# Optimization experiments

Hardware: AMD Instinct MI355X
Metric: run time of the kernel (lower is better)

## Reference

```python
import math
import jax
import jax.numpy as jnp
import numpy as np

N_NODE = 50000
N_EDGE = 1_600_000
D_IN = 128
D_K = 32
N_HEADS = 8


def setup_inputs() -> dict:
    key = jax.random.key(0)
    k_h, k_e, k_q, k_k, k_v = jax.random.split(key, 5)
    h = jax.random.normal(k_h, (N_NODE, D_IN), dtype=jnp.float32)
    edge_idx = jax.random.randint(k_e, (2, N_EDGE), 0, N_NODE, dtype=jnp.int64)
    scale = 1.0 / math.sqrt(D_IN)
    WQ = jax.random.normal(k_q, (N_HEADS, D_IN, D_K), dtype=jnp.float32) * scale
    WK = jax.random.normal(k_k, (N_HEADS, D_IN, D_K), dtype=jnp.float32) * scale
    WV = jax.random.normal(k_v, (N_HEADS, D_IN, D_K), dtype=jnp.float32) * scale
    return {"h": h, "edge_idx": edge_idx, "WQ": WQ, "WK": WK, "WV": WV}


def reference(h, edge_idx, WQ, WK, WV):
    n_node = h.shape[0]
    d_k = WK.shape[-1]
    # Per-head projections: [H, N, d]
    Q = jnp.einsum('nd,hdk->hnk', h, WQ)
    K = jnp.einsum('nd,hdk->hnk', h, WK)
    V = jnp.einsum('nd,hdv->hnv', h, WV)
    row = edge_idx[0]  # destination (softmax normalized per row, dim=1)
    col = edge_idx[1]  # source
    # Edge logits: e[h, e] = <Q[h, row[e]], K[h, col[e]]> / sqrt(d_k)
    e = jnp.einsum('hek,hek->he', Q[:, row, :], K[:, col, :]) / jnp.sqrt(
        jnp.asarray(d_k, dtype=h.dtype))
    eT = e.T  # [E, H]
    # Sparse (segment) softmax over outgoing edges of each row node.
    m = jax.ops.segment_max(eT, row, num_segments=n_node)  # [N, H]
    m = jnp.where(jnp.isfinite(m), m, jnp.zeros_like(m))   # guard empty rows
    ex = jnp.exp(eT - m[row])                               # [E, H]
    denom = jax.ops.segment_sum(ex, row, num_segments=n_node)  # [N, H]
    att = ex / denom[row]                                   # [E, H]
    # Sparse mm: out[i] = sum_{edges (i,j)} att * V[j]
    msgs = att[:, :, None] * jnp.transpose(V, (1, 0, 2))[col]  # [E, H, d_v]
    out = jax.ops.segment_sum(msgs, row, num_segments=n_node)  # [N, H, d_v]
    # aggregate == 'concat' -> head-major concat along feature dim
    return out.reshape(n_node, -1)
```

## Files before the change

### kernel.cpp

```cpp
#include <hip/hip_runtime.h>
#include <hip/hip_bf16.h>
#include <cstdint>

#define D_IN 128
#define DK 32
#define NH 8
#define HD 256

typedef __attribute__((ext_vector_type(8))) short short8;
typedef __attribute__((ext_vector_type(4))) float f32x4;

__device__ inline float bf2f(unsigned short u) {
  union { unsigned int i; float f; } c;
  c.i = ((unsigned int)u) << 16;
  return c.f;
}
__device__ inline short f2bf(float f) {
  union { float f; unsigned int i; } c; c.f = f;
  unsigned int u = c.i;
  u = u + 0x7FFFu + ((u >> 16) & 1u);
  return (short)(u >> 16);
}

__global__ __launch_bounds__(256) void prep_w_kernel(
    const float* __restrict__ WQ, const float* __restrict__ WK,
    const float* __restrict__ WV, short8* __restrict__ Bbuf) {
  int ct = blockIdx.x;
  int t = threadIdx.x;
  int kt = t >> 6, L = t & 63;
  int col = ct * 16 + (L & 15);
  int type = col >> 8;
  const float* W = (type == 0) ? WQ : (type == 1) ? WK : WV;
  int head = (col & 255) >> 5;
  int kk = col & 31;
  int k0 = kt * 32 + ((L >> 4) << 3);
  short8 o;
  #pragma unroll
  for (int r = 0; r < 8; r++)
    o[r] = f2bf(W[head * (D_IN * DK) + (k0 + r) * DK + kk]);
  Bbuf[(size_t)(ct * 4 + kt) * 64 + L] = o;
}

__global__ __launch_bounds__(256) void gemm_qkv_kernel(
    const float* __restrict__ h, const short8* __restrict__ Bbuf,
    __hip_bfloat16* __restrict__ Q, __hip_bfloat16* __restrict__ K,
    __hip_bfloat16* __restrict__ V, int nt_total) {
  __shared__ float hs[16][132];
  __shared__ short lds[16][768];
  int nt = blockIdx.x;
  int t = threadIdx.x;
  {
    const float4* h4 = (const float4*)(h + (size_t)nt * 16 * 128);
    float4 v0 = h4[t * 2], v1 = h4[t * 2 + 1];
    int node = t >> 4, dim = (t & 15) * 8;
    hs[node][dim + 0] = v0.x; hs[node][dim + 1] = v0.y;
    hs[node][dim + 2] = v0.z; hs[node][dim + 3] = v0.w;
    hs[node][dim + 4] = v1.x; hs[node][dim + 5] = v1.y;
    hs[node][dim + 6] = v1.z; hs[node][dim + 7] = v1.w;
  }
  __syncthreads();
  int w = t >> 6;
  int L = t & 63;
  int arow = L & 15, k0base = ((L >> 4) << 3);
  short8 afrag[4];
  #pragma unroll
  for (int kt = 0; kt < 4; kt++) {
    #pragma unroll
    for (int r = 0; r < 8; r++)
      afrag[kt][r] = f2bf(hs[arow][kt * 32 + k0base + r]);
  }
  f32x4 acc[12];
  #pragma unroll
  for (int c = 0; c < 12; c++) acc[c] = (f32x4){0.f, 0.f, 0.f, 0.f};
  #pragma unroll
  for (int kt = 0; kt < 4; kt++) {
    #pragma unroll
    for (int c = 0; c < 12; c++) {
      short8 b = Bbuf[(size_t)((w * 12 + c) * 4 + kt) * 64 + L];
      acc[c] = __builtin_amdgcn_mfma_f32_16x16x32_bf16(afrag[kt], b, acc[c], 0, 0, 0);
    }
  }
  int row0 = (L >> 4) << 2;
  int col0 = w * 192 + (L & 15);
  #pragma unroll
  for (int c = 0; c < 12; c++) {
    #pragma unroll
    for (int r = 0; r < 4; r++)
      lds[row0 + r][col0 + c * 16] = f2bf(acc[c][r]);
  }
  __syncthreads();
  __hip_bfloat16* dst[3] = {Q, K, V};
  #pragma unroll
  for (int s = 0; s < 3; s++) {
    char* base = (char*)(dst[s] + (size_t)nt * 16 * HD);
    #pragma unroll
    for (int j = 0; j < 2; j++) {
      int u = t + j * 256;
      int row = u >> 5, uc = u & 31;
      float4 vdat = *(const float4*)((const char*)&lds[row][0] + s * 512 + uc * 16);
      *(float4*)(base + row * 512 + uc * 16) = vdat;
    }
  }
}

__global__ void rank_kernel(const int* __restrict__ row, int n_edge,
                            int* __restrict__ cnt, int* __restrict__ rank) {
  int i = blockIdx.x * blockDim.x + threadIdx.x;
  if (i < n_edge) rank[i] = atomicAdd(&cnt[row[i]], 1);
}

__global__ __launch_bounds__(256) void scan1_kernel(
    const int* __restrict__ cnt, int n, int* __restrict__ exc,
    int* __restrict__ bsum) {
  __shared__ int s[256];
  int gid = blockIdx.x * 256 + threadIdx.x;
  int v = (gid < n) ? cnt[gid] : 0;
  s[threadIdx.x] = v;
  __syncthreads();
  #pragma unroll
  for (int off = 1; off < 256; off <<= 1) {
    int t = (threadIdx.x >= off) ? s[threadIdx.x - off] : 0;
    __syncthreads();
    s[threadIdx.x] += t;
    __syncthreads();
  }
  if (gid < n) exc[gid] = s[threadIdx.x] - v;
  if (threadIdx.x == 255) bsum[blockIdx.x] = s[255];
}

__global__ __launch_bounds__(256) void scan2_kernel(int* __restrict__ bsum,
                                                    int nb) {
  __shared__ int s[256];
  int v = (threadIdx.x < nb) ? bsum[threadIdx.x] : 0;
  s[threadIdx.x] = v;
  __syncthreads();
  #pragma unroll
  for (int off = 1; off < 256; off <<= 1) {
    int t = (threadIdx.x >= off) ? s[threadIdx.x - off] : 0;
    __syncthreads();
    s[threadIdx.x] += t;
    __syncthreads();
  }
  if (threadIdx.x < nb) bsum[threadIdx.x] = s[threadIdx.x] - v;
}

__global__ __launch_bounds__(256) void scan3_kernel(
    int* __restrict__ exc, const int* __restrict__ bsum, int n, int n_edge) {
  int gid = blockIdx.x * 256 + threadIdx.x;
  if (gid < n) exc[gid] = exc[gid] + bsum[blockIdx.x];
  if (gid == 0) exc[n] = n_edge;
}

__global__ void scatter_kernel(const int* __restrict__ row,
                               const int* __restrict__ col,
                               const int* __restrict__ rank, int n_edge,
                               const int* __restrict__ offsets,
                               int* __restrict__ col_sorted) {
  int i = blockIdx.x * blockDim.x + threadIdx.x;
  if (i < n_edge) col_sorted[offsets[row[i]] + rank[i]] = col[i];
}

__global__ __launch_bounds__(256) void attn_kernel(
    const __hip_bfloat16* __restrict__ Q, const __hip_bfloat16* __restrict__ K,
    const __hip_bfloat16* __restrict__ V, const int* __restrict__ offsets,
    const int* __restrict__ col_sorted, float* __restrict__ out, int n_node) {
  int wave = threadIdx.x >> 6;
  int lane = threadIdx.x & 63;
  int node = blockIdx.x * 4 + wave;
  if (node >= n_node) return;
  int start = offsets[node], end = offsets[node + 1];
  int d0 = lane * 4;

  float q0, q1, q2, q3;
  {
    ushort4 qv = *(const ushort4*)(Q + (size_t)node * HD + d0);
    q0 = bf2f(qv.x); q1 = bf2f(qv.y); q2 = bf2f(qv.z); q3 = bf2f(qv.w);
  }
  float m = -INFINITY, denom = 0.f;
  float a0 = 0.f, a1 = 0.f, a2 = 0.f, a3 = 0.f;

  for (int e = start; e < end; e += 2) {
    int c0 = col_sorted[e];
    bool has1 = (e + 1 < end);
    int c1 = has1 ? col_sorted[e + 1] : c0;
    ushort4 k0 = *(const ushort4*)(K + (size_t)c0 * HD + d0);
    ushort4 v0 = *(const ushort4*)(V + (size_t)c0 * HD + d0);
    ushort4 k1 = *(const ushort4*)(K + (size_t)c1 * HD + d0);
    ushort4 v1 = *(const ushort4*)(V + (size_t)c1 * HD + d0);
    {
      float d = q0 * bf2f(k0.x) + q1 * bf2f(k0.y) + q2 * bf2f(k0.z) +
                q3 * bf2f(k0.w);
      d += __shfl_xor(d, 1);
      d += __shfl_xor(d, 2);
      d += __shfl_xor(d, 4);
      float lg = d * 0.17677669529663687f;
      float nm = fmaxf(m, lg);
      float sc = __expf(m - nm);
      float p = __expf(lg - nm);
      denom = denom * sc + p;
      a0 = a0 * sc + p * bf2f(v0.x);
      a1 = a1 * sc + p * bf2f(v0.y);
      a2 = a2 * sc + p * bf2f(v0.z);
      a3 = a3 * sc + p * bf2f(v0.w);
      m = nm;
    }
    if (has1) {
      float d = q0 * bf2f(k1.x) + q1 * bf2f(k1.y) + q2 * bf2f(k1.z) +
                q3 * bf2f(k1.w);
      d += __shfl_xor(d, 1);
      d += __shfl_xor(d, 2);
      d += __shfl_xor(d, 4);
      float lg = d * 0.17677669529663687f;
      float nm = fmaxf(m, lg);
      float sc = __expf(m - nm);
      float p = __expf(lg - nm);
      denom = denom * sc + p;
      a0 = a0 * sc + p * bf2f(v1.x);
      a1 = a1 * sc + p * bf2f(v1.y);
      a2 = a2 * sc + p * bf2f(v1.z);
      a3 = a3 * sc + p * bf2f(v1.w);
      m = nm;
    }
  }
  float inv = (end > start) ? 1.f / denom : 0.f;
  float4 o = make_float4(a0 * inv, a1 * inv, a2 * inv, a3 * inv);
  *(float4*)(out + (size_t)node * HD + d0) = o;
}

extern "C" void kernel_launch(void* const* d_in, const int* in_sizes, int n_in,
                              void* d_out, int out_size, void* d_ws,
                              size_t ws_size, hipStream_t stream) {
  const float* h = (const float*)d_in[0];
  const int* edge = (const int*)d_in[1];
  const float* WQ = (const float*)d_in[2];
  const float* WK = (const float*)d_in[3];
  const float* WV = (const float*)d_in[4];
  float* out = (float*)d_out;

  int n_node = in_sizes[0] / D_IN;
  int n_edge = in_sizes[1] / 2;
  const int* row = edge;
  const int* col = edge + n_edge;

  char* ws = (char*)d_ws;
  size_t off = 0;
  auto alloc = [&](size_t bytes) {
    void* p = ws + off;
    off += (bytes + 255) & ~(size_t)255;
    return p;
  };
  int nt_total = (n_node + 15) / 16;
  __hip_bfloat16* Q = (__hip_bfloat16*)alloc((size_t)nt_total * 16 * HD * 2);
  __hip_bfloat16* K = (__hip_bfloat16*)alloc((size_t)nt_total * 16 * HD * 2);
  __hip_bfloat16* V = (__hip_bfloat16*)alloc((size_t)nt_total * 16 * HD * 2);
  short8* Bbuf = (short8*)alloc((size_t)48 * 4 * 64 * 16);
  int* col_sorted = (int*)alloc((size_t)n_edge * 4);
  int* rank = (int*)alloc((size_t)n_edge * 4);
  int* cnt = (int*)alloc((size_t)n_node * 4);
  int* offsets = (int*)alloc((size_t)(n_node + 1) * 4);
  int* bsum = (int*)alloc(256 * 4);

  hipMemsetAsync(cnt, 0, (size_t)n_node * 4, stream);

  prep_w_kernel<<<48, 256, 0, stream>>>(WQ, WK, WV, Bbuf);
  gemm_qkv_kernel<<<nt_total, 256, 0, stream>>>(h, Bbuf, Q, K, V, nt_total);

  int nb_e = (n_edge + 255) / 256;
  rank_kernel<<<nb_e, 256, 0, stream>>>(row, n_edge, cnt, rank);

  int nb = (n_node + 255) / 256;
  scan1_kernel<<<nb, 256, 0, stream>>>(cnt, n_node, offsets, bsum);
  scan2_kernel<<<1, 256, 0, stream>>>(bsum, nb);
  scan3_kernel<<<nb, 256, 0, stream>>>(offsets, bsum, n_node, n_edge);

  scatter_kernel<<<nb_e, 256, 0, stream>>>(row, col, rank, n_edge, offsets,
                                           col_sorted);

  attn_kernel<<<(n_node + 3) / 4, 256, 0, stream>>>(Q, K, V, offsets,
                                                    col_sorted, out, n_node);
}
```

Before: 379.5 us.

## Interleave K and V rows and use lazy-rescale online softmax

New measurement: 376.9 us. About the same (-0.7%).

```diff
diff --git a/kernel.cpp b/kernel.cpp
--- a/kernel.cpp
+++ b/kernel.cpp
@@ -6,6 +6,7 @@
 #define DK 32
 #define NH 8
 #define HD 256
+#define KVW 512
 
 typedef __attribute__((ext_vector_type(8))) short short8;
 typedef __attribute__((ext_vector_type(4))) float f32x4;
@@ -14,6 +15,9 @@
   union { unsigned int i; float f; } c;
   c.i = ((unsigned int)u) << 16;
   return c.f;
+}
+__device__ inline float u2f(unsigned int u) {
+  union { unsigned int i; float f; } c; c.i = u; return c.f;
 }
 __device__ inline short f2bf(float f) {
   union { float f; unsigned int i; } c; c.f = f;
@@ -43,8 +47,8 @@
 
 __global__ __launch_bounds__(256) void gemm_qkv_kernel(
     const float* __restrict__ h, const short8* __restrict__ Bbuf,
-    __hip_bfloat16* __restrict__ Q, __hip_bfloat16* __restrict__ K,
-    __hip_bfloat16* __restrict__ V, int nt_total) {
+    __hip_bfloat16* __restrict__ Q, __hip_bfloat16* __restrict__ KV,
+    int nt_total) {
   __shared__ float hs[16][132];
   __shared__ short lds[16][768];
   int nt = blockIdx.x;
@@ -89,17 +93,19 @@
       lds[row0 + r][col0 + c * 16] = f2bf(acc[c][r]);
   }
   __syncthreads();
-  __hip_bfloat16* dst[3] = {Q, K, V};
-  #pragma unroll
-  for (int s = 0; s < 3; s++) {
-    char* base = (char*)(dst[s] + (size_t)nt * 16 * HD);
-    #pragma unroll
-    for (int j = 0; j < 2; j++) {
-      int u = t + j * 256;
-      int row = u >> 5, uc = u & 31;
-      float4 vdat = *(const float4*)((const char*)&lds[row][0] + s * 512 + uc * 16);
-      *(float4*)(base + row * 512 + uc * 16) = vdat;
-    }
+  #pragma unroll
+  for (int j = 0; j < 2; j++) {
+    int u = t + j * 256;
+    int row = u >> 5, uc = u & 31;
+    float4 vdat = *(const float4*)&lds[row][uc * 8];
+    *(float4*)(Q + (size_t)(nt * 16 + row) * HD + uc * 8) = vdat;
+  }
+  #pragma unroll
+  for (int j = 0; j < 4; j++) {
+    int u = t + j * 256;
+    int row = u >> 6, uc = u & 63;
+    float4 vdat = *(const float4*)&lds[row][256 + uc * 8];
+    *(float4*)(KV + (size_t)(nt * 16 + row) * KVW + uc * 8) = vdat;
   }
 }
 
@@ -160,71 +166,87 @@
   if (i < n_edge) col_sorted[offsets[row[i]] + rank[i]] = col[i];
 }
 
+#define AT_PROCESS(r)                                                        \
+  {                                                                          \
+    float x0 = u2f(r.x << 16), x1 = u2f(r.x & 0xFFFF0000u);                  \
+    float x2 = u2f(r.y << 16), x3 = u2f(r.y & 0xFFFF0000u);                  \
+    float x4 = u2f(r.z << 16), x5 = u2f(r.z & 0xFFFF0000u);                  \
+    float x6 = u2f(r.w << 16), x7 = u2f(r.w & 0xFFFF0000u);                  \
+    float d = x0 * qf0;                                                      \
+    d = fmaf(x1, qf1, d); d = fmaf(x2, qf2, d); d = fmaf(x3, qf3, d);        \
+    d = fmaf(x4, qf4, d); d = fmaf(x5, qf5, d); d = fmaf(x6, qf6, d);        \
+    d = fmaf(x7, qf7, d);                                                    \
+    d += __shfl_xor(d, 1);                                                   \
+    d += __shfl_xor(d, 2);                                                   \
+    float lg = __shfl(d, sub);                                               \
+    if (__any(lg - m > 8.0f)) {                                              \
+      float nm = fmaxf(m, lg);                                               \
+      float sc = __expf(m - nm);                                             \
+      denom *= sc;                                                           \
+      a0 *= sc; a1 *= sc; a2 *= sc; a3 *= sc;                                \
+      a4 *= sc; a5 *= sc; a6 *= sc; a7 *= sc;                                \
+      m = nm;                                                                \
+    }                                                                        \
+    float p = __expf(lg - m);                                                \
+    denom += p;                                                              \
+    a0 = fmaf(p, x0, a0); a1 = fmaf(p, x1, a1);                              \
+    a2 = fmaf(p, x2, a2); a3 = fmaf(p, x3, a3);                              \
+    a4 = fmaf(p, x4, a4); a5 = fmaf(p, x5, a5);                              \
+    a6 = fmaf(p, x6, a6); a7 = fmaf(p, x7, a7);                              \
+  }
+
 __global__ __launch_bounds__(256) void attn_kernel(
-    const __hip_bfloat16* __restrict__ Q, const __hip_bfloat16* __restrict__ K,
-    const __hip_bfloat16* __restrict__ V, const int* __restrict__ offsets,
-    const int* __restrict__ col_sorted, float* __restrict__ out, int n_node) {
+    const __hip_bfloat16* __restrict__ Q, const __hip_bfloat16* __restrict__ KV,
+    const int* __restrict__ offsets, const int* __restrict__ col_sorted,
+    float* __restrict__ out, int n_node) {
   int wave = threadIdx.x >> 6;
   int lane = threadIdx.x & 63;
+  int sub = lane & 31;
   int node = blockIdx.x * 4 + wave;
   if (node >= n_node) return;
   int start = offsets[node], end = offsets[node + 1];
-  int d0 = lane * 4;
-
-  float q0, q1, q2, q3;
+
+  const float QS = 0.17677669529663687f;
+  float qf0, qf1, qf2, qf3, qf4, qf5, qf6, qf7;
   {
-    ushort4 qv = *(const ushort4*)(Q + (size_t)node * HD + d0);
-    q0 = bf2f(qv.x); q1 = bf2f(qv.y); q2 = bf2f(qv.z); q3 = bf2f(qv.w);
+    uint4 qr = *(const uint4*)(Q + (size_t)node * HD + sub * 8);
+    qf0 = u2f(qr.x << 16) * QS; qf1 = u2f(qr.x & 0xFFFF0000u) * QS;
+    qf2 = u2f(qr.y << 16) * QS; qf3 = u2f(qr.y & 0xFFFF0000u) * QS;
+    qf4 = u2f(qr.z << 16) * QS; qf5 = u2f(qr.z & 0xFFFF0000u) * QS;
+    qf6 = u2f(qr.w << 16) * QS; qf7 = u2f(qr.w & 0xFFFF0000u) * QS;
   }
   float m = -INFINITY, denom = 0.f;
   float a0 = 0.f, a1 = 0.f, a2 = 0.f, a3 = 0.f;
-
-  for (int e = start; e < end; e += 2) {
-    int c0 = col_sorted[e];
-    bool has1 = (e + 1 < end);
-    int c1 = has1 ? col_sorted[e + 1] : c0;
-    ushort4 k0 = *(const ushort4*)(K + (size_t)c0 * HD + d0);
-    ushort4 v0 = *(const ushort4*)(V + (size_t)c0 * HD + d0);
-    ushort4 k1 = *(const ushort4*)(K + (size_t)c1 * HD + d0);
-    ushort4 v1 = *(const ushort4*)(V + (size_t)c1 * HD + d0);
-    {
-      float d = q0 * bf2f(k0.x) + q1 * bf2f(k0.y) + q2 * bf2f(k0.z) +
-                q3 * bf2f(k0.w);
-      d += __shfl_xor(d, 1);
-      d += __shfl_xor(d, 2);
-      d += __shfl_xor(d, 4);
-      float lg = d * 0.17677669529663687f;
-      float nm = fmaxf(m, lg);
-      float sc = __expf(m - nm);
-      float p = __expf(lg - nm);
-      denom = denom * sc + p;
-      a0 = a0 * sc + p * bf2f(v0.x);
-      a1 = a1 * sc + p * bf2f(v0.y);
-      a2 = a2 * sc + p * bf2f(v0.z);
-      a3 = a3 * sc + p * bf2f(v0.w);
-      m = nm;
-    }
-    if (has1) {
-      float d = q0 * bf2f(k1.x) + q1 * bf2f(k1.y) + q2 * bf2f(k1.z) +
-                q3 * bf2f(k1.w);
-      d += __shfl_xor(d, 1);
-      d += __shfl_xor(d, 2);
-      d += __shfl_xor(d, 4);
-      float lg = d * 0.17677669529663687f;
-      float nm = fmaxf(m, lg);
-      float sc = __expf(m - nm);
-      float p = __expf(lg - nm);
-      denom = denom * sc + p;
-      a0 = a0 * sc + p * bf2f(v1.x);
-      a1 = a1 * sc + p * bf2f(v1.y);
-      a2 = a2 * sc + p * bf2f(v1.z);
-      a3 = a3 * sc + p * bf2f(v1.w);
-      m = nm;
-    }
-  }
+  float a4 = 0.f, a5 = 0.f, a6 = 0.f, a7 = 0.f;
+
+  const char* kvbase = (const char*)KV + lane * 16;
+  int e = start;
+  for (; e + 4 <= end; e += 4) {
+    int c0 = col_sorted[e], c1 = col_sorted[e + 1];
+    int c2 = col_sorted[e + 2], c3 = col_sorted[e + 3];
+    uint4 r0 = *(const uint4*)(kvbase + (size_t)c0 * 1024);
+    uint4 r1 = *(const uint4*)(kvbase + (size_t)c1 * 1024);
+    uint4 r2 = *(const uint4*)(kvbase + (size_t)c2 * 1024);
+    uint4 r3 = *(const uint4*)(kvbase + (size_t)c3 * 1024);
+    AT_PROCESS(r0);
+    AT_PROCESS(r1);
+    AT_PROCESS(r2);
+    AT_PROCESS(r3);
+  }
+  for (; e < end; e++) {
+    int c = col_sorted[e];
+    uint4 r = *(const uint4*)(kvbase + (size_t)c * 1024);
+    AT_PROCESS(r);
+  }
+
   float inv = (end > start) ? 1.f / denom : 0.f;
-  float4 o = make_float4(a0 * inv, a1 * inv, a2 * inv, a3 * inv);
-  *(float4*)(out + (size_t)node * HD + d0) = o;
+  if (lane >= 32) {
+    float* op = out + (size_t)node * HD + sub * 8;
+    float4 o0 = make_float4(a0 * inv, a1 * inv, a2 * inv, a3 * inv);
+    float4 o1 = make_float4(a4 * inv, a5 * inv, a6 * inv, a7 * inv);
+    *(float4*)op = o0;
+    *(float4*)(op + 4) = o1;
+  }
 }
 
 extern "C" void kernel_launch(void* const* d_in, const int* in_sizes, int n_in,
@@ -251,8 +273,7 @@
   };
   int nt_total = (n_node + 15) / 16;
   __hip_bfloat16* Q = (__hip_bfloat16*)alloc((size_t)nt_total * 16 * HD * 2);
-  __hip_bfloat16* K = (__hip_bfloat16*)alloc((size_t)nt_total * 16 * HD * 2);
-  __hip_bfloat16* V = (__hip_bfloat16*)alloc((size_t)nt_total * 16 * HD * 2);
+  __hip_bfloat16* KV = (__hip_bfloat16*)alloc((size_t)nt_total * 16 * KVW * 2);
   short8* Bbuf = (short8*)alloc((size_t)48 * 4 * 64 * 16);
   int* col_sorted = (int*)alloc((size_t)n_edge * 4);
   int* rank = (int*)alloc((size_t)n_edge * 4);
@@ -263,7 +284,7 @@
   hipMemsetAsync(cnt, 0, (size_t)n_node * 4, stream);
 
   prep_w_kernel<<<48, 256, 0, stream>>>(WQ, WK, WV, Bbuf);
-  gemm_qkv_kernel<<<nt_total, 256, 0, stream>>>(h, Bbuf, Q, K, V, nt_total);
+  gemm_qkv_kernel<<<nt_total, 256, 0, stream>>>(h, Bbuf, Q, KV, nt_total);
 
   int nb_e = (n_edge + 255) / 256;
   rank_kernel<<<nb_e, 256, 0, stream>>>(row, n_edge, cnt, rank);
@@ -276,6 +297,6 @@
   scatter_kernel<<<nb_e, 256, 0, stream>>>(row, col, rank, n_edge, offsets,
                                            col_sorted);
 
-  attn_kernel<<<(n_node + 3) / 4, 256, 0, stream>>>(Q, K, V, offsets,
-                                                    col_sorted, out, n_node);
-}
+  attn_kernel<<<(n_node + 3) / 4, 256, 0, stream>>>(Q, KV, offsets, col_sorted,
+                                                    out, n_node);
+}
```
